# Kernel optimization log

Measured on AMD Instinct MI355X. Metric: run time of the kernel, lower is better.

Reference implementation:

```python
import jax, jax.numpy as jnp
import numpy as np

B, S, E = 2, 2048, 1024
H = 16
A = 1024
DH = A // H  # 64 per-head attention dim


def setup_inputs() -> dict:
    key = jax.random.key(0)
    ks = jax.random.split(key, 9)
    s = lambda fan_in: 1.0 / np.sqrt(fan_in)
    return {
        "x": jax.random.normal(ks[0], (B, S, E), dtype=jnp.float32),
        # per-head Q/K/V projections stacked over heads: [H, E, DH]
        "Wq": jax.random.normal(ks[1], (H, E, DH), dtype=jnp.float32) * s(E),
        "bq": jnp.zeros((H, DH), dtype=jnp.float32),
        "Wk": jax.random.normal(ks[2], (H, E, DH), dtype=jnp.float32) * s(E),
        "bk": jnp.zeros((H, DH), dtype=jnp.float32),
        "Wv": jax.random.normal(ks[3], (H, E, DH), dtype=jnp.float32) * s(E),
        "bv": jnp.zeros((H, DH), dtype=jnp.float32),
        # output projection Linear(A, E): stored as [A, E]
        "Wo": jax.random.normal(ks[4], (A, E), dtype=jnp.float32) * s(A),
        "bo": jnp.zeros((E,), dtype=jnp.float32),
    }


def reference(x, Wq, bq, Wk, bk, Wv, bv, Wo, bo):
    # Batched equivalent of the per-head Python loop:
    # each head: q = x Wq_h + bq_h ; scores = q k^T / sqrt(DH) ; softmax ; @ v
    q = jnp.einsum("bse,hed->bhsd", x, Wq) + bq[None, :, None, :]
    k = jnp.einsum("bse,hed->bhsd", x, Wk) + bk[None, :, None, :]
    v = jnp.einsum("bse,hed->bhsd", x, Wv) + bv[None, :, None, :]
    scale = 1.0 / jnp.sqrt(jnp.asarray(DH, dtype=x.dtype))
    scores = jnp.einsum("bhsd,bhtd->bhst", q, k) * scale  # [B,H,S,S]
    attn = jax.nn.softmax(scores, axis=-1)
    heads = jnp.einsum("bhst,bhtd->bhsd", attn, v)  # [B,H,S,DH]
    # concat heads along last dim (matches torch.cat over head outputs)
    concat = heads.transpose(0, 2, 1, 3).reshape(x.shape[0], x.shape[1], H * DH)
    return concat @ Wo + bo  # final Linear(dim_attention, dim_embedding)
```

## Files before the change

kernel.cpp:

```cpp
#include <hip/hip_runtime.h>
#include <math.h>


namespace {
constexpr int kBn = 2, kS = 2048, kE = 1024, kH = 16, kDH = 64, kA = 1024;

typedef __attribute__((ext_vector_type(8))) short short8;
typedef __attribute__((ext_vector_type(4))) float f32x4;

#define QSCALE 0.18033688011112042f

__device__ inline unsigned short f2bf(float f) {
  union { float f; unsigned u; } x; x.f = f;
  unsigned r = x.u + 0x7fffu + ((x.u >> 16) & 1u);
  return (unsigned short)(r >> 16);
}

__device__ inline void gld16(const void* g, void* l) {
  __builtin_amdgcn_global_load_lds(
      (const __attribute__((address_space(1))) unsigned int*)g,
      (__attribute__((address_space(3))) unsigned int*)l, 16, 0, 0);
}

__global__ __launch_bounds__(256) void cast_x_kernel(
    const float* __restrict__ x, unsigned short* __restrict__ xb) {
  const int i = (blockIdx.x * 256 + threadIdx.x) * 8;
  float4 a = *(const float4*)(x + i);
  float4 b = *(const float4*)(x + i + 4);
  unsigned short t[8];
  t[0] = f2bf(a.x); t[1] = f2bf(a.y); t[2] = f2bf(a.z); t[3] = f2bf(a.w);
  t[4] = f2bf(b.x); t[5] = f2bf(b.y); t[6] = f2bf(b.z); t[7] = f2bf(b.w);
  *(short8*)(xb + i) = *(const short8*)t;
}

__global__ __launch_bounds__(256) void cast_wqkv_kernel(
    const float* __restrict__ Wq, const float* __restrict__ Wk,
    const float* __restrict__ Wv, unsigned short* __restrict__ Wt) {
  const int sel = blockIdx.z;
  const float* __restrict__ W = (sel == 0) ? Wq : (sel == 1) ? Wk : Wv;
  const int h = blockIdx.y;
  const int e0 = blockIdx.x * 64;
  const int tid = threadIdx.x;

  __shared__ float T[64][68];
  const int el = tid >> 2, dq = tid & 3;
  const float* src = W + ((size_t)h * kE + e0 + el) * kDH + dq * 16;
#pragma unroll
  for (int j = 0; j < 4; ++j)
    *(float4*)&T[el][dq * 16 + j * 4] = *(const float4*)(src + j * 4);
  __syncthreads();

  const int d = tid & 63, w = tid >> 6;
  unsigned short t[16];
#pragma unroll
  for (int j = 0; j < 16; ++j) t[j] = f2bf(T[w * 16 + j][d]);
  unsigned short* dst =
      Wt + (((size_t)sel << 20) | ((size_t)(h * 64 + d) << 10)) + e0 + w * 16;
  *(short8*)dst = *(const short8*)&t[0];
  *(short8*)(dst + 8) = *(const short8*)&t[8];
}

__global__ __launch_bounds__(256) void cast_wo_kernel(
    const float* __restrict__ Wo, unsigned short* __restrict__ Wot) {
  const int a0 = blockIdx.x * 64, e0 = blockIdx.y * 64;
  const int tid = threadIdx.x;

  __shared__ float T[64][68];
  const int al = tid >> 2, dq = tid & 3;
  const float* src = Wo + (size_t)(a0 + al) * kE + e0 + dq * 16;
#pragma unroll
  for (int j = 0; j < 4; ++j)
    *(float4*)&T[al][dq * 16 + j * 4] = *(const float4*)(src + j * 4);
  __syncthreads();

  const int e = tid & 63, w = tid >> 6;
  unsigned short t[16];
#pragma unroll
  for (int j = 0; j < 16; ++j) t[j] = f2bf(T[w * 16 + j][e]);
  unsigned short* dst = Wot + ((size_t)(e0 + e) << 10) + a0 + w * 16;
  *(short8*)dst = *(const short8*)&t[0];
  *(short8*)(dst + 8) = *(const short8*)&t[8];
}

__global__ __launch_bounds__(256) void gemm_bf16_kernel(
    const unsigned short* __restrict__ A, const unsigned short* __restrict__ Bt,
    const float* __restrict__ b0, const float* __restrict__ b1,
    const float* __restrict__ b2,
    unsigned short* __restrict__ oq, unsigned short* __restrict__ okk,
    unsigned short* __restrict__ ov, float* __restrict__ of, int modeBase) {
  constexpr int K = 1024;
  const int mode = modeBase ? 3 : (int)blockIdx.z;
  const unsigned short* Bm = Bt + ((size_t)(modeBase ? 0 : blockIdx.z) << 20);
  const float* bias = (mode == 1) ? b1 : (mode == 2) ? b2 : b0;

  const int mt = blockIdx.x, nt = blockIdx.y;
  const int tid = threadIdx.x;
  const int wv = tid >> 6, lane = tid & 63, lq = lane & 15, quad = lane >> 4;
  const int wm = wv >> 1, wn = wv & 1;

  __shared__ unsigned short lA[128 * 32];
  __shared__ unsigned short lB[128 * 32];

  const int c0 = wv * 64 + lane;
  const int c1 = c0 + 256;
  const unsigned short* gA0 = A + (size_t)(mt * 128 + (c0 >> 2)) * K + (c0 & 3) * 8;
  const unsigned short* gA1 = A + (size_t)(mt * 128 + (c1 >> 2)) * K + (c1 & 3) * 8;
  const unsigned short* gB0 = Bm + (size_t)(nt * 128 + (c0 >> 2)) * K + (c0 & 3) * 8;
  const unsigned short* gB1 = Bm + (size_t)(nt * 128 + (c1 >> 2)) * K + (c1 & 3) * 8;
  unsigned short* lA0 = lA + (size_t)(wv * 64) * 8;
  unsigned short* lA1 = lA0 + 256 * 8;
  unsigned short* lB0 = lB + (size_t)(wv * 64) * 8;
  unsigned short* lB1 = lB0 + 256 * 8;

  f32x4 acc[4][4];
#pragma unroll
  for (int i = 0; i < 4; ++i)
#pragma unroll
    for (int j = 0; j < 4; ++j) acc[i][j] = (f32x4){0.f, 0.f, 0.f, 0.f};

  for (int k0 = 0; k0 < K; k0 += 32) {
    gld16(gA0 + k0, lA0);
    gld16(gA1 + k0, lA1);
    gld16(gB0 + k0, lB0);
    gld16(gB1 + k0, lB1);
    __syncthreads();
    short8 af[4], bfr[4];
#pragma unroll
    for (int i = 0; i < 4; ++i)
      af[i] = *(const short8*)&lA[(wm * 64 + i * 16 + lq) * 32 + quad * 8];
#pragma unroll
    for (int j = 0; j < 4; ++j)
      bfr[j] = *(const short8*)&lB[(wn * 64 + j * 16 + lq) * 32 + quad * 8];
#pragma unroll
    for (int i = 0; i < 4; ++i)
#pragma unroll
      for (int j = 0; j < 4; ++j)
        acc[i][j] = __builtin_amdgcn_mfma_f32_16x16x32_bf16(af[i], bfr[j],
                                                            acc[i][j], 0, 0, 0);
    __syncthreads();
  }

  const int n0 = nt * 128 + wn * 64;
  float bv4[4];
#pragma unroll
  for (int j = 0; j < 4; ++j) bv4[j] = bias[n0 + j * 16 + lq];

  if (mode == 3) {
    const int m0 = mt * 128 + wm * 64;
#pragma unroll
    for (int i = 0; i < 4; ++i)
#pragma unroll
      for (int j = 0; j < 4; ++j)
#pragma unroll
        for (int r = 0; r < 4; ++r)
          of[(size_t)(m0 + i * 16 + quad * 4 + r) * kE + n0 + j * 16 + lq] =
              acc[i][j][r] + bv4[j];
  } else {
    const int tok0 = mt * 128 + wm * 64;
    const int b = tok0 >> 11;
    const int s0 = tok0 & (kS - 1);
    const int h = n0 >> 6;
    if (mode < 2) {
      unsigned short* o = (mode == 0) ? oq : okk;
      const float scl = (mode == 0) ? QSCALE : 1.0f;
#pragma unroll
      for (int i = 0; i < 4; ++i)
#pragma unroll
        for (int j = 0; j < 4; ++j) {
          const int d = j * 16 + lq;
#pragma unroll
          for (int r = 0; r < 4; ++r) {
            const int s = s0 + i * 16 + quad * 4 + r;
            o[((size_t)(b * kH + h) * kS + s) * kDH + d] =
                f2bf((acc[i][j][r] + bv4[j]) * scl);
          }
        }
    } else {
#pragma unroll
      for (int i = 0; i < 4; ++i)
#pragma unroll
        for (int j = 0; j < 4; ++j) {
          const int d = j * 16 + lq;
          union { unsigned short u[4]; uint2 v; } pk;
#pragma unroll
          for (int r = 0; r < 4; ++r) pk.u[r] = f2bf(acc[i][j][r] + bv4[j]);
          const int s = s0 + i * 16 + quad * 4;
          *(uint2*)(ov + ((size_t)(b * kH + h) * kDH + d) * kS + s) = pk.v;
        }
    }
  }
}

#define QT 128
#define KT 64
#define LDK 72
__global__ __launch_bounds__(256) void attn_mfma_kernel(
    const unsigned short* __restrict__ q, const unsigned short* __restrict__ k,
    const unsigned short* __restrict__ vt, unsigned short* __restrict__ cc) {
  const int bh = blockIdx.y;
  const int b = bh >> 4, h = bh & 15;
  const int tid = threadIdx.x;
  const int wv = tid >> 6;
  const int lane = tid & 63;
  const int lq = lane & 15;
  const int quad = lane >> 4;

  __shared__ unsigned short Ks[KT][LDK];
  __shared__ unsigned short Vt[kDH][LDK];
  __shared__ unsigned short Pb[QT][LDK];

  const int q0 = blockIdx.x * QT;

  short8 qa[2][2];
#pragma unroll
  for (int mf = 0; mf < 2; ++mf) {
    const unsigned short* qbase =
        q + ((size_t)bh * kS + q0 + wv * 32 + mf * 16 + lq) * kDH;
    qa[mf][0] = *(const short8*)(qbase + quad * 8);
    qa[mf][1] = *(const short8*)(qbase + 32 + quad * 8);
  }

  f32x4 Oacc[2][4];
  f32x4 Osum[2];
#pragma unroll
  for (int mf = 0; mf < 2; ++mf) {
    Osum[mf] = (f32x4){0.f, 0.f, 0.f, 0.f};
#pragma unroll
    for (int dt = 0; dt < 4; ++dt) Oacc[mf][dt] = (f32x4){0.f, 0.f, 0.f, 0.f};
  }

  unsigned short ob[8];
#pragma unroll
  for (int i = 0; i < 8; ++i) ob[i] = 0x3F80;
  const short8 ones = *(const short8*)ob;

  const unsigned short* kg = k + (size_t)bh * kS * kDH;
  const unsigned short* vg = vt + (size_t)bh * kDH * kS;

  for (int t0 = 0; t0 < kS; t0 += KT) {
    __syncthreads();
#pragma unroll
    for (int p = 0; p < 2; ++p) {
      const int id = p * 256 + tid;
      const int row = id >> 3, c = (id & 7) << 3;
      *(short8*)&Ks[row][c] = *(const short8*)(kg + (size_t)(t0 + row) * kDH + c);
      *(short8*)&Vt[row][c] = *(const short8*)(vg + (size_t)row * kS + t0 + c);
    }
    __syncthreads();

    f32x4 S[2][4];
#pragma unroll
    for (int nt = 0; nt < 4; ++nt) {
      short8 kb0 = *(const short8*)&Ks[nt * 16 + lq][quad * 8];
      short8 kb1 = *(const short8*)&Ks[nt * 16 + lq][32 + quad * 8];
#pragma unroll
      for (int mf = 0; mf < 2; ++mf) {
        f32x4 acc = (f32x4){0.f, 0.f, 0.f, 0.f};
        acc = __builtin_amdgcn_mfma_f32_16x16x32_bf16(qa[mf][0], kb0, acc, 0, 0, 0);
        acc = __builtin_amdgcn_mfma_f32_16x16x32_bf16(qa[mf][1], kb1, acc, 0, 0, 0);
        S[mf][nt] = acc;
      }
    }

#pragma unroll
    for (int mf = 0; mf < 2; ++mf)
#pragma unroll
      for (int nt = 0; nt < 4; ++nt)
#pragma unroll
        for (int r = 0; r < 4; ++r) {
          const float p = __builtin_amdgcn_exp2f(S[mf][nt][r]);
          union { float f; unsigned u; } x; x.f = p;
          Pb[wv * 32 + mf * 16 + quad * 4 + r][nt * 16 + lq] =
              (unsigned short)((x.u + 0x8000u) >> 16);
        }

    short8 pa[2][2];
#pragma unroll
    for (int mf = 0; mf < 2; ++mf) {
      pa[mf][0] = *(const short8*)&Pb[wv * 32 + mf * 16 + lq][quad * 8];
      pa[mf][1] = *(const short8*)&Pb[wv * 32 + mf * 16 + lq][32 + quad * 8];
    }

#pragma unroll
    for (int dt = 0; dt < 4; ++dt) {
      short8 vb0 = *(const short8*)&Vt[dt * 16 + lq][quad * 8];
      short8 vb1 = *(const short8*)&Vt[dt * 16 + lq][32 + quad * 8];
#pragma unroll
      for (int mf = 0; mf < 2; ++mf) {
        Oacc[mf][dt] =
            __builtin_amdgcn_mfma_f32_16x16x32_bf16(pa[mf][0], vb0, Oacc[mf][dt], 0, 0, 0);
        Oacc[mf][dt] =
            __builtin_amdgcn_mfma_f32_16x16x32_bf16(pa[mf][1], vb1, Oacc[mf][dt], 0, 0, 0);
      }
    }
#pragma unroll
    for (int mf = 0; mf < 2; ++mf) {
      Osum[mf] = __builtin_amdgcn_mfma_f32_16x16x32_bf16(pa[mf][0], ones, Osum[mf], 0, 0, 0);
      Osum[mf] = __builtin_amdgcn_mfma_f32_16x16x32_bf16(pa[mf][1], ones, Osum[mf], 0, 0, 0);
    }
  }

#pragma unroll
  for (int mf = 0; mf < 2; ++mf)
#pragma unroll
    for (int r = 0; r < 4; ++r) {
      const float inv = 1.0f / Osum[mf][r];
      const int qrow = q0 + wv * 32 + mf * 16 + quad * 4 + r;
      unsigned short* base = cc + ((size_t)b * kS + qrow) * kA + h * kDH;
#pragma unroll
      for (int dt = 0; dt < 4; ++dt) base[dt * 16 + lq] = f2bf(Oacc[mf][dt][r] * inv);
    }
}

}

extern "C" void kernel_launch(void* const* d_in, const int* in_sizes, int n_in,
                              void* d_out, int out_size, void* d_ws, size_t ws_size,
                              hipStream_t stream) {
  const float* x  = (const float*)d_in[0];
  const float* Wq = (const float*)d_in[1];
  const float* bq = (const float*)d_in[2];
  const float* Wk = (const float*)d_in[3];
  const float* bk = (const float*)d_in[4];
  const float* Wv = (const float*)d_in[5];
  const float* bv = (const float*)d_in[6];
  const float* Wo = (const float*)d_in[7];
  const float* bo = (const float*)d_in[8];
  float* out = (float*)d_out;

  const size_t per = (size_t)kBn * kH * kS * kDH;
  unsigned short* xb  = (unsigned short*)d_ws;
  unsigned short* qb  = xb + per;
  unsigned short* kb  = qb + per;
  unsigned short* vtb = kb + per;
  unsigned short* cc  = vtb + per;
  unsigned short* Wt  = cc + per;
  unsigned short* Wot = Wt + 3 * (per / 4);

  cast_x_kernel<<<dim3(per / (256 * 8)), 256, 0, stream>>>(x, xb);
  cast_wqkv_kernel<<<dim3(16, 16, 3), 256, 0, stream>>>(Wq, Wk, Wv, Wt);
  cast_wo_kernel<<<dim3(16, 16), 256, 0, stream>>>(Wo, Wot);

  gemm_bf16_kernel<<<dim3(32, 8, 3), 256, 0, stream>>>(
      xb, Wt, bq, bk, bv, qb, kb, vtb, nullptr, 0);

  attn_mfma_kernel<<<dim3(kS / QT, kBn * kH), 256, 0, stream>>>(qb, kb, vtb, cc);

  gemm_bf16_kernel<<<dim3(32, 8, 1), 256, 0, stream>>>(
      cc, Wot, bo, nullptr, nullptr, nullptr, nullptr, nullptr, out, 1);
}
```

Measured before the change: 227.5 us.

## Split attention over two key halves and merge partial outputs in a new kernel

The attention kernel gains a third grid dimension that splits the key/value sequence into two halves. Each half writes unnormalized bf16 partial outputs plus row sums, and a new merge kernel adds the halves, normalizes and scatters them into the concatenated head layout. This doubles the number of attention blocks to fill the GPU better. In exchange it adds an extra kernel launch, extra global traffic for the partial buffers, and an intermediate bf16 rounding of the unnormalized partials.

```diff
diff --git a/kernel.cpp b/kernel.cpp
--- a/kernel.cpp
+++ b/kernel.cpp
@@ -4,6 +4,7 @@
 
 namespace {
 constexpr int kBn = 2, kS = 2048, kE = 1024, kH = 16, kDH = 64, kA = 1024;
+constexpr int kRows = kBn * kH * kS;
 
 typedef __attribute__((ext_vector_type(8))) short short8;
 typedef __attribute__((ext_vector_type(4))) float f32x4;
@@ -14,6 +15,11 @@
   union { float f; unsigned u; } x; x.f = f;
   unsigned r = x.u + 0x7fffu + ((x.u >> 16) & 1u);
   return (unsigned short)(r >> 16);
+}
+
+__device__ inline float bf2f(unsigned short s) {
+  union { unsigned u; float f; } x; x.u = ((unsigned)s) << 16;
+  return x.f;
 }
 
 __device__ inline void gld16(const void* g, void* l) {
@@ -196,9 +202,11 @@
 #define LDK 72
 __global__ __launch_bounds__(256) void attn_mfma_kernel(
     const unsigned short* __restrict__ q, const unsigned short* __restrict__ k,
-    const unsigned short* __restrict__ vt, unsigned short* __restrict__ cc) {
+    const unsigned short* __restrict__ vt,
+    unsigned short* __restrict__ Op0, unsigned short* __restrict__ Op1,
+    float* __restrict__ Ssum) {
   const int bh = blockIdx.y;
-  const int b = bh >> 4, h = bh & 15;
+  const int split = blockIdx.z;
   const int tid = threadIdx.x;
   const int wv = tid >> 6;
   const int lane = tid & 63;
@@ -237,7 +245,8 @@
   const unsigned short* kg = k + (size_t)bh * kS * kDH;
   const unsigned short* vg = vt + (size_t)bh * kDH * kS;
 
-  for (int t0 = 0; t0 < kS; t0 += KT) {
+  const int tEnd = split * 1024 + 1024;
+  for (int t0 = split * 1024; t0 < tEnd; t0 += KT) {
     __syncthreads();
 #pragma unroll
     for (int p = 0; p < 2; ++p) {
@@ -300,16 +309,38 @@
     }
   }
 
+  unsigned short* Op = split ? Op1 : Op0;
+  const size_t rbase = (size_t)bh * kS;
 #pragma unroll
   for (int mf = 0; mf < 2; ++mf)
 #pragma unroll
     for (int r = 0; r < 4; ++r) {
-      const float inv = 1.0f / Osum[mf][r];
       const int qrow = q0 + wv * 32 + mf * 16 + quad * 4 + r;
-      unsigned short* base = cc + ((size_t)b * kS + qrow) * kA + h * kDH;
-#pragma unroll
-      for (int dt = 0; dt < 4; ++dt) base[dt * 16 + lq] = f2bf(Oacc[mf][dt][r] * inv);
-    }
+      unsigned short* base = Op + (rbase + qrow) * kDH;
+#pragma unroll
+      for (int dt = 0; dt < 4; ++dt) base[dt * 16 + lq] = f2bf(Oacc[mf][dt][r]);
+      if (lq == 0) Ssum[(size_t)split * kRows + rbase + qrow] = Osum[mf][r];
+    }
+}
+
+__global__ __launch_bounds__(256) void merge_kernel(
+    const unsigned short* __restrict__ Op0, const unsigned short* __restrict__ Op1,
+    const float* __restrict__ Ssum, unsigned short* __restrict__ cc) {
+  const int gid = blockIdx.x * 256 + threadIdx.x;
+  const int row = gid >> 3;
+  const int d0 = (gid & 7) * 8;
+
+  const float inv = 1.0f / (Ssum[row] + Ssum[kRows + row]);
+
+  union { short8 v; unsigned short u[8]; } a, b, o;
+  a.v = *(const short8*)(Op0 + (size_t)row * kDH + d0);
+  b.v = *(const short8*)(Op1 + (size_t)row * kDH + d0);
+#pragma unroll
+  for (int j = 0; j < 8; ++j) o.u[j] = f2bf((bf2f(a.u[j]) + bf2f(b.u[j])) * inv);
+
+  const int bh = row >> 11, s = row & (kS - 1);
+  const int bb = bh >> 4, h = bh & 15;
+  *(short8*)(cc + ((size_t)(bb * kS + s) * kA) + h * kDH + d0) = o.v;
 }
 
 }
@@ -336,6 +367,9 @@
   unsigned short* cc  = vtb + per;
   unsigned short* Wt  = cc + per;
   unsigned short* Wot = Wt + 3 * (per / 4);
+  unsigned short* Op1 = Wot + (per / 4);
+  float* Ssum = (float*)(Op1 + per);
+  unsigned short* Op0 = xb;
 
   cast_x_kernel<<<dim3(per / (256 * 8)), 256, 0, stream>>>(x, xb);
   cast_wqkv_kernel<<<dim3(16, 16, 3), 256, 0, stream>>>(Wq, Wk, Wv, Wt);
@@ -344,7 +378,10 @@
   gemm_bf16_kernel<<<dim3(32, 8, 3), 256, 0, stream>>>(
       xb, Wt, bq, bk, bv, qb, kb, vtb, nullptr, 0);
 
-  attn_mfma_kernel<<<dim3(kS / QT, kBn * kH), 256, 0, stream>>>(qb, kb, vtb, cc);
+  attn_mfma_kernel<<<dim3(kS / QT, kBn * kH, 2), 256, 0, stream>>>(
+      qb, kb, vtb, Op0, Op1, Ssum);
+
+  merge_kernel<<<dim3(kRows * 8 / 256), 256, 0, stream>>>(Op0, Op1, Ssum, cc);
 
   gemm_bf16_kernel<<<dim3(32, 8, 1), 256, 0, stream>>>(
       cc, Wot, bo, nullptr, nullptr, nullptr, nullptr, nullptr, out, 1);
```

New measurement: 232.0 us. About the same (+2.0%).
